# Kernel tuning notes

Measured on AMD Instinct MI355X. Metric: run time of the kernel, lower is better.

## Reference

```python
import jax, jax.numpy as jnp
import numpy as np


def setup_inputs() -> dict:
    key = jax.random.key(0)
    k1, k2 = jax.random.split(key)
    B, P, N, M = 8, 32, 1024, 1024
    normalized_receptive_fields = jax.random.normal(k1, (B, P, N, 3), dtype=jnp.float32)
    reconstructed_points = jax.random.normal(k2, (B, P, M, 3), dtype=jnp.float32)
    return {
        "normalized_receptive_fields": normalized_receptive_fields,
        "reconstructed_points": reconstructed_points,
    }


def reference(normalized_receptive_fields, reconstructed_points):
    B, P, M, _ = reconstructed_points.shape
    N = normalized_receptive_fields.shape[2]
    # Faithful to torch: permute(0,1,3,2) then reshape(-1, M, 3).
    x = jnp.transpose(reconstructed_points, (0, 1, 3, 2)).reshape(-1, M, 3)  # (BP, M, 3)
    y = normalized_receptive_fields.reshape(-1, N, 3)                        # (BP, N, 3)
    xx = jnp.sum(x * x, axis=-1)                 # (BP, M)
    yy = jnp.sum(y * y, axis=-1)                 # (BP, N)
    xy = jnp.einsum('bmc,bnc->bmn', x, y)        # (BP, M, N)
    dist = xx[:, :, None] + yy[:, None, :] - 2.0 * xy  # (BP, M, N)
    min_x_to_y = jnp.min(dist, axis=2)           # (BP, M)
    min_y_to_x = jnp.min(dist, axis=1)           # (BP, N)
    return jnp.mean(min_x_to_y) + jnp.mean(min_y_to_x)
```

## Files before the change

### kernel.cpp

```cpp
#include <hip/hip_runtime.h>


#define MM 1024
#define NN 1024
#define THREADS 1024
#define NWAVES 16
#define FINF 3.4e38f

typedef float f32x4 __attribute__((ext_vector_type(4)));
typedef __bf16 bf16x8 __attribute__((ext_vector_type(8)));

#define BT_OFF 0
#define CK_OFF 65536
#define RS_OFF (CK_OFF + 8192)
#define LDS_BYTES (RS_OFF + 64)

__device__ __forceinline__ unsigned short bf16_rne(float v) {
    unsigned u = __float_as_uint(v);
    u = u + 0x7FFFu + ((u >> 16) & 1u);
    return (unsigned short)(u >> 16);
}
__device__ __forceinline__ float bf16f(unsigned short h) {
    return __uint_as_float(((unsigned)h) << 16);
}
struct S3 { unsigned short h0, h1, h2; };
__device__ __forceinline__ S3 split3(float v) {
    S3 o;
    o.h0 = bf16_rne(v);
    float r = v - bf16f(o.h0);
    o.h1 = bf16_rne(r);
    float r2 = r - bf16f(o.h1);
    o.h2 = bf16_rne(r2);
    return o;
}
__device__ __forceinline__ unsigned pk(unsigned short a, unsigned short b) {
    return (unsigned)a | ((unsigned)b << 16);
}
__device__ __forceinline__ float min3f(float a, float b, float c) {
    return fminf(fminf(a, b), c);
}
template <int CTRL>
__device__ __forceinline__ float dpp_ror_min(float v) {
    int vi = __float_as_int(v);
    int t  = __builtin_amdgcn_update_dpp(vi, vi, CTRL, 0xf, 0xf, true);
    return fminf(v, __int_as_float(t));
}
__device__ __forceinline__ unsigned fkey(float v) {
    unsigned u = __float_as_uint(v);
    return ((int)u < 0) ? ~u : (u | 0x80000000u);
}
__device__ __forceinline__ float unkey(unsigned k) {
    return ((int)k < 0) ? __uint_as_float(k & 0x7FFFFFFFu) : __uint_as_float(~k);
}

__global__ __launch_bounds__(THREADS, 8)
void chamfer_main(const float* __restrict__ nrf,
                  const float* __restrict__ rp,
                  float* __restrict__ colP,
                  float* __restrict__ out,
                  float inv_bpm) {
    __shared__ __align__(16) unsigned char smem[LDS_BYTES];
    unsigned* colK = (unsigned*)(smem + CK_OFF);
    float* rowsumS = (float*)(smem + RS_OFF);

    const int bp   = blockIdx.x >> 1;
    const int half = blockIdx.x & 1;
    const int tid  = threadIdx.x;
    const int lane = tid & 63;
    const int wave = tid >> 6;
    const int l15  = lane & 15;
    const int g    = lane >> 4;
    const unsigned short ONE = 0x3F80;

    const float* yB = nrf + (size_t)bp * NN * 3;
    const float* xB = rp + (size_t)bp * MM * 3;

    {
        const int c = tid;
        float y0 = yB[c * 3 + 0], y1 = yB[c * 3 + 1], y2 = yB[c * 3 + 2];
        float yy = __builtin_fmaf(y0, y0, __builtin_fmaf(y1, y1, y2 * y2));
        S3 b0 = split3(y0), b1 = split3(y1), b2 = split3(y2), q = split3(yy);
        uint4* dst = (uint4*)(smem + BT_OFF + (c >> 4) * 1024 + (c & 15) * 64);
        dst[0] = make_uint4(pk(b0.h0, b0.h1), pk(b0.h0, b0.h1), pk(b0.h2, b0.h0), pk(b1.h0, b1.h1));
        dst[1] = make_uint4(pk(b1.h0, b1.h1), pk(b1.h2, b1.h0), pk(b2.h0, b2.h1), pk(b2.h0, b2.h1));
        dst[2] = make_uint4(pk(b2.h2, b2.h0), pk(ONE, ONE), pk(ONE, q.h0), pk(q.h1, q.h2));
        dst[3] = make_uint4(pk(b0.h2, b0.h1), pk(b1.h2, b1.h1), pk(b2.h2, b2.h1), 0u);
        colK[c] = 0xFFFFFFFFu;
        colK[1024 + c] = 0xFFFFFFFFu;
    }

    bf16x8 af[2];
    #pragma unroll
    for (int s = 0; s < 2; ++s) {
        const int m = half * 512 + wave * 32 + s * 16 + l15;
        const int k = 3 * m;
        float x0 = xB[((k    ) & (MM - 1)) * 3 + ((k    ) >> 10)];
        float x1 = xB[((k + 1) & (MM - 1)) * 3 + ((k + 1) >> 10)];
        float x2 = xB[((k + 2) & (MM - 1)) * 3 + ((k + 2) >> 10)];
        float xx = __builtin_fmaf(x0, x0, __builtin_fmaf(x1, x1, x2 * x2));
        S3 a0 = split3(-2.0f * x0), a1 = split3(-2.0f * x1), a2 = split3(-2.0f * x2);
        S3 p = split3(xx);
        uint4 q0 = make_uint4(pk(a0.h0, a0.h0), pk(a0.h1, a0.h1), pk(a0.h0, a0.h2), pk(a1.h0, a1.h0));
        uint4 q1 = make_uint4(pk(a1.h1, a1.h1), pk(a1.h0, a1.h2), pk(a2.h0, a2.h0), pk(a2.h1, a2.h1));
        uint4 q2 = make_uint4(pk(a2.h0, a2.h2), pk(p.h0, p.h1), pk(p.h2, ONE), pk(ONE, ONE));
        uint4 q3 = make_uint4(pk(a0.h1, a0.h2), pk(a1.h1, a1.h2), pk(a2.h1, a2.h2), 0u);
        uint4 sel = (g == 0) ? q0 : (g == 1) ? q1 : (g == 2) ? q2 : q3;
        union { uint4 u; bf16x8 b; } cv; cv.u = sel;
        af[s] = cv.b;
    }
    __syncthreads();

    const unsigned fragoff = (unsigned)((l15 * 4 + g) * 16);
    const unsigned char* BtBase = smem + BT_OFF;
    unsigned* colKme = colK + (lane >> 5) * 1024 + l15;
    const f32x4 Z = {0.0f, 0.0f, 0.0f, 0.0f};

    float rmin0[4], rmin1[4];
    #pragma unroll
    for (int j = 0; j < 4; ++j) { rmin0[j] = FINF; rmin1[j] = FINF; }

    bf16x8 bfc = *(const bf16x8*)(BtBase + fragoff);
    #pragma unroll
    for (int t = 0; t < 64; ++t) {
        bf16x8 bfn = *(const bf16x8*)(BtBase + (t + 1) * 1024 + fragoff);

        f32x4 acc0 = __builtin_amdgcn_mfma_f32_16x16x32_bf16(af[0], bfc, Z, 0, 0, 0);
        f32x4 acc1 = __builtin_amdgcn_mfma_f32_16x16x32_bf16(af[1], bfc, Z, 0, 0, 0);

        #pragma unroll
        for (int j = 0; j < 4; ++j) rmin0[j] = fminf(rmin0[j], acc0[j]);
        #pragma unroll
        for (int j = 0; j < 4; ++j) rmin1[j] = fminf(rmin1[j], acc1[j]);

        float cm0 = fminf(min3f(acc0[0], acc0[1], acc0[2]), acc0[3]);
        float cm1 = fminf(min3f(acc1[0], acc1[1], acc1[2]), acc1[3]);
        float cm = fminf(cm0, cm1);
        int sw = __builtin_amdgcn_ds_swizzle(__float_as_int(cm), 0x401F);
        cm = fminf(cm, __int_as_float(sw));
        atomicMin(colKme + t * 16, fkey(cm));

        bfc = bfn;
    }

    float rowsum = 0.0f;
    #pragma unroll
    for (int s = 0; s < 2; ++s) {
        #pragma unroll
        for (int j = 0; j < 4; ++j) {
            float v = (s == 0) ? rmin0[j] : rmin1[j];
            v = dpp_ror_min<0x121>(v);
            v = dpp_ror_min<0x122>(v);
            v = dpp_ror_min<0x124>(v);
            v = dpp_ror_min<0x128>(v);
            rowsum += v;
        }
    }
    rowsum += __int_as_float(__builtin_amdgcn_ds_swizzle(__float_as_int(rowsum), 0x401F));
    rowsum += __int_as_float(__builtin_amdgcn_ds_bpermute((lane ^ 32) << 2, __float_as_int(rowsum)));
    if (lane == 0) rowsumS[wave] = rowsum;
    __syncthreads();

    {
        unsigned k0 = colK[tid], k1 = colK[1024 + tid];
        colP[(size_t)blockIdx.x * 1024 + tid] = unkey(k0 < k1 ? k0 : k1);
    }
    if (tid < 64) {
        float r = (tid < 16) ? rowsumS[tid] : 0.0f;
        #pragma unroll
        for (int off = 8; off > 0; off >>= 1) r += __shfl_xor(r, off, 64);
        if (tid == 0) atomicAdd(out, r * inv_bpm);
    }
}

__global__ __launch_bounds__(1024)
void chamfer_reduce(const float* __restrict__ colP, float* __restrict__ out,
                    float inv_bpn) {
    const int bp = blockIdx.x;
    const int tid = threadIdx.x;
    const int lane = tid & 63;
    const int wave = tid >> 6;
    __shared__ float ws[16];

    float v = fminf(colP[(size_t)(2 * bp) * 1024 + tid],
                    colP[(size_t)(2 * bp + 1) * 1024 + tid]);
    #pragma unroll
    for (int off = 32; off > 0; off >>= 1) v += __shfl_xor(v, off, 64);
    if (lane == 0) ws[wave] = v;
    __syncthreads();
    if (tid == 0) {
        float s = 0.0f;
        #pragma unroll
        for (int w = 0; w < 16; ++w) s += ws[w];
        atomicAdd(out, s * inv_bpn);
    }
}

extern "C" void kernel_launch(void* const* d_in, const int* in_sizes, int n_in,
                              void* d_out, int out_size, void* d_ws, size_t ws_size,
                              hipStream_t stream) {
    const float* nrf = (const float*)d_in[0];
    const float* rp  = (const float*)d_in[1];
    float* out = (float*)d_out;
    float* colP = (float*)d_ws;

    const int BP = in_sizes[1] / (MM * 3);
    const float inv_bpm = 1.0f / (float)(BP * MM);
    const float inv_bpn = 1.0f / (float)(BP * NN);

    (void)hipMemsetAsync(out, 0, sizeof(float), stream);
    chamfer_main<<<BP * 2, THREADS, 0, stream>>>(nrf, rp, colP, out, inv_bpm);
    chamfer_reduce<<<BP, 1024, 0, stream>>>(colP, out, inv_bpn);
}
```

Before: 89.45 us.

## Compute both chamfer directions as row-min passes and drop column atomics and reduce kernel

Instead of splitting the M rows across two blocks and tracking column minima with LDS atomicMin, each block pair now computes one direction: block 0 does rows of x against y, block 1 does rows of y against x, each using only register row-min reductions. This removes the per-tile swizzle and atomicMin on LDS, the colP workspace round-trip, and the second reduce kernel launch. In exchange it doubles the total MFMA work, since each distance matrix is computed twice, and raises register use with four A fragments per wave.

New measurement: 126.8 us. 41.7% more time.

```diff
diff --git a/kernel.cpp b/kernel.cpp
--- a/kernel.cpp
+++ b/kernel.cpp
@@ -11,8 +11,8 @@
 typedef __bf16 bf16x8 __attribute__((ext_vector_type(8)));
 
 #define BT_OFF 0
-#define CK_OFF 65536
-#define RS_OFF (CK_OFF + 8192)
+#define PAD_OFF 65536
+#define RS_OFF (PAD_OFF + 1024)
 #define LDS_BYTES (RS_OFF + 64)
 
 __device__ __forceinline__ unsigned short bf16_rne(float v) {
@@ -36,35 +36,23 @@
 __device__ __forceinline__ unsigned pk(unsigned short a, unsigned short b) {
     return (unsigned)a | ((unsigned)b << 16);
 }
-__device__ __forceinline__ float min3f(float a, float b, float c) {
-    return fminf(fminf(a, b), c);
-}
 template <int CTRL>
 __device__ __forceinline__ float dpp_ror_min(float v) {
     int vi = __float_as_int(v);
     int t  = __builtin_amdgcn_update_dpp(vi, vi, CTRL, 0xf, 0xf, true);
     return fminf(v, __int_as_float(t));
 }
-__device__ __forceinline__ unsigned fkey(float v) {
-    unsigned u = __float_as_uint(v);
-    return ((int)u < 0) ? ~u : (u | 0x80000000u);
-}
-__device__ __forceinline__ float unkey(unsigned k) {
-    return ((int)k < 0) ? __uint_as_float(k & 0x7FFFFFFFu) : __uint_as_float(~k);
-}
 
 __global__ __launch_bounds__(THREADS, 8)
 void chamfer_main(const float* __restrict__ nrf,
                   const float* __restrict__ rp,
-                  float* __restrict__ colP,
                   float* __restrict__ out,
-                  float inv_bpm) {
+                  float inv_bpm, float inv_bpn) {
     __shared__ __align__(16) unsigned char smem[LDS_BYTES];
-    unsigned* colK = (unsigned*)(smem + CK_OFF);
     float* rowsumS = (float*)(smem + RS_OFF);
 
     const int bp   = blockIdx.x >> 1;
-    const int half = blockIdx.x & 1;
+    const int dir  = blockIdx.x & 1;
     const int tid  = threadIdx.x;
     const int lane = tid & 63;
     const int wave = tid >> 6;
@@ -77,29 +65,40 @@
 
     {
         const int c = tid;
-        float y0 = yB[c * 3 + 0], y1 = yB[c * 3 + 1], y2 = yB[c * 3 + 2];
-        float yy = __builtin_fmaf(y0, y0, __builtin_fmaf(y1, y1, y2 * y2));
-        S3 b0 = split3(y0), b1 = split3(y1), b2 = split3(y2), q = split3(yy);
+        float v0, v1, v2;
+        if (dir == 0) {
+            v0 = yB[c * 3 + 0]; v1 = yB[c * 3 + 1]; v2 = yB[c * 3 + 2];
+        } else {
+            const int k = 3 * c;
+            v0 = xB[((k    ) & (MM - 1)) * 3 + ((k    ) >> 10)];
+            v1 = xB[((k + 1) & (MM - 1)) * 3 + ((k + 1) >> 10)];
+            v2 = xB[((k + 2) & (MM - 1)) * 3 + ((k + 2) >> 10)];
+        }
+        float nn = __builtin_fmaf(v0, v0, __builtin_fmaf(v1, v1, v2 * v2));
+        S3 b0 = split3(v0), b1 = split3(v1), b2 = split3(v2), q = split3(nn);
         uint4* dst = (uint4*)(smem + BT_OFF + (c >> 4) * 1024 + (c & 15) * 64);
         dst[0] = make_uint4(pk(b0.h0, b0.h1), pk(b0.h0, b0.h1), pk(b0.h2, b0.h0), pk(b1.h0, b1.h1));
         dst[1] = make_uint4(pk(b1.h0, b1.h1), pk(b1.h2, b1.h0), pk(b2.h0, b2.h1), pk(b2.h0, b2.h1));
         dst[2] = make_uint4(pk(b2.h2, b2.h0), pk(ONE, ONE), pk(ONE, q.h0), pk(q.h1, q.h2));
         dst[3] = make_uint4(pk(b0.h2, b0.h1), pk(b1.h2, b1.h1), pk(b2.h2, b2.h1), 0u);
-        colK[c] = 0xFFFFFFFFu;
-        colK[1024 + c] = 0xFFFFFFFFu;
     }
 
-    bf16x8 af[2];
+    bf16x8 af[4];
     #pragma unroll
-    for (int s = 0; s < 2; ++s) {
-        const int m = half * 512 + wave * 32 + s * 16 + l15;
-        const int k = 3 * m;
-        float x0 = xB[((k    ) & (MM - 1)) * 3 + ((k    ) >> 10)];
-        float x1 = xB[((k + 1) & (MM - 1)) * 3 + ((k + 1) >> 10)];
-        float x2 = xB[((k + 2) & (MM - 1)) * 3 + ((k + 2) >> 10)];
-        float xx = __builtin_fmaf(x0, x0, __builtin_fmaf(x1, x1, x2 * x2));
-        S3 a0 = split3(-2.0f * x0), a1 = split3(-2.0f * x1), a2 = split3(-2.0f * x2);
-        S3 p = split3(xx);
+    for (int s = 0; s < 4; ++s) {
+        const int m = wave * 64 + s * 16 + l15;
+        float v0, v1, v2;
+        if (dir == 0) {
+            const int k = 3 * m;
+            v0 = xB[((k    ) & (MM - 1)) * 3 + ((k    ) >> 10)];
+            v1 = xB[((k + 1) & (MM - 1)) * 3 + ((k + 1) >> 10)];
+            v2 = xB[((k + 2) & (MM - 1)) * 3 + ((k + 2) >> 10)];
+        } else {
+            v0 = yB[m * 3 + 0]; v1 = yB[m * 3 + 1]; v2 = yB[m * 3 + 2];
+        }
+        float nn = __builtin_fmaf(v0, v0, __builtin_fmaf(v1, v1, v2 * v2));
+        S3 a0 = split3(-2.0f * v0), a1 = split3(-2.0f * v1), a2 = split3(-2.0f * v2);
+        S3 p = split3(nn);
         uint4 q0 = make_uint4(pk(a0.h0, a0.h0), pk(a0.h1, a0.h1), pk(a0.h0, a0.h2), pk(a1.h0, a1.h0));
         uint4 q1 = make_uint4(pk(a1.h1, a1.h1), pk(a1.h0, a1.h2), pk(a2.h0, a2.h0), pk(a2.h1, a2.h1));
         uint4 q2 = make_uint4(pk(a2.h0, a2.h2), pk(p.h0, p.h1), pk(p.h2, ONE), pk(ONE, ONE));
@@ -110,44 +109,41 @@
     }
     __syncthreads();
 
-    const unsigned fragoff = (unsigned)((l15 * 4 + g) * 16);
-    const unsigned char* BtBase = smem + BT_OFF;
-    unsigned* colKme = colK + (lane >> 5) * 1024 + l15;
+    const unsigned char* BtBase = smem + BT_OFF + (unsigned)((l15 * 4 + g) * 16);
     const f32x4 Z = {0.0f, 0.0f, 0.0f, 0.0f};
 
-    float rmin0[4], rmin1[4];
+    float rmin[4][4];
     #pragma unroll
-    for (int j = 0; j < 4; ++j) { rmin0[j] = FINF; rmin1[j] = FINF; }
+    for (int s = 0; s < 4; ++s)
+        #pragma unroll
+        for (int j = 0; j < 4; ++j) rmin[s][j] = FINF;
 
-    bf16x8 bfc = *(const bf16x8*)(BtBase + fragoff);
+    bf16x8 bfc = *(const bf16x8*)(BtBase);
     #pragma unroll
     for (int t = 0; t < 64; ++t) {
-        bf16x8 bfn = *(const bf16x8*)(BtBase + (t + 1) * 1024 + fragoff);
+        bf16x8 bfn = *(const bf16x8*)(BtBase + (t + 1) * 1024);
 
         f32x4 acc0 = __builtin_amdgcn_mfma_f32_16x16x32_bf16(af[0], bfc, Z, 0, 0, 0);
         f32x4 acc1 = __builtin_amdgcn_mfma_f32_16x16x32_bf16(af[1], bfc, Z, 0, 0, 0);
+        f32x4 acc2 = __builtin_amdgcn_mfma_f32_16x16x32_bf16(af[2], bfc, Z, 0, 0, 0);
+        f32x4 acc3 = __builtin_amdgcn_mfma_f32_16x16x32_bf16(af[3], bfc, Z, 0, 0, 0);
 
         #pragma unroll
-        for (int j = 0; j < 4; ++j) rmin0[j] = fminf(rmin0[j], acc0[j]);
-        #pragma unroll
-        for (int j = 0; j < 4; ++j) rmin1[j] = fminf(rmin1[j], acc1[j]);
-
-        float cm0 = fminf(min3f(acc0[0], acc0[1], acc0[2]), acc0[3]);
-        float cm1 = fminf(min3f(acc1[0], acc1[1], acc1[2]), acc1[3]);
-        float cm = fminf(cm0, cm1);
-        int sw = __builtin_amdgcn_ds_swizzle(__float_as_int(cm), 0x401F);
-        cm = fminf(cm, __int_as_float(sw));
-        atomicMin(colKme + t * 16, fkey(cm));
-
+        for (int j = 0; j < 4; ++j) {
+            rmin[0][j] = fminf(rmin[0][j], acc0[j]);
+            rmin[1][j] = fminf(rmin[1][j], acc1[j]);
+            rmin[2][j] = fminf(rmin[2][j], acc2[j]);
+            rmin[3][j] = fminf(rmin[3][j], acc3[j]);
+        }
         bfc = bfn;
     }
 
     float rowsum = 0.0f;
     #pragma unroll
-    for (int s = 0; s < 2; ++s) {
+    for (int s = 0; s < 4; ++s) {
         #pragma unroll
         for (int j = 0; j < 4; ++j) {
-            float v = (s == 0) ? rmin0[j] : rmin1[j];
+            float v = rmin[s][j];
             v = dpp_ror_min<0x121>(v);
             v = dpp_ror_min<0x122>(v);
             v = dpp_ror_min<0x124>(v);
@@ -160,38 +156,11 @@
     if (lane == 0) rowsumS[wave] = rowsum;
     __syncthreads();
 
-    {
-        unsigned k0 = colK[tid], k1 = colK[1024 + tid];
-        colP[(size_t)blockIdx.x * 1024 + tid] = unkey(k0 < k1 ? k0 : k1);
-    }
     if (tid < 64) {
-        float r = (tid < 16) ? rowsumS[tid] : 0.0f;
+        float r = (tid < NWAVES) ? rowsumS[tid] : 0.0f;
         #pragma unroll
         for (int off = 8; off > 0; off >>= 1) r += __shfl_xor(r, off, 64);
-        if (tid == 0) atomicAdd(out, r * inv_bpm);
-    }
-}
-
-__global__ __launch_bounds__(1024)
-void chamfer_reduce(const float* __restrict__ colP, float* __restrict__ out,
-                    float inv_bpn) {
-    const int bp = blockIdx.x;
-    const int tid = threadIdx.x;
-    const int lane = tid & 63;
-    const int wave = tid >> 6;
-    __shared__ float ws[16];
-
-    float v = fminf(colP[(size_t)(2 * bp) * 1024 + tid],
-                    colP[(size_t)(2 * bp + 1) * 1024 + tid]);
-    #pragma unroll
-    for (int off = 32; off > 0; off >>= 1) v += __shfl_xor(v, off, 64);
-    if (lane == 0) ws[wave] = v;
-    __syncthreads();
-    if (tid == 0) {
-        float s = 0.0f;
-        #pragma unroll
-        for (int w = 0; w < 16; ++w) s += ws[w];
-        atomicAdd(out, s * inv_bpn);
+        if (tid == 0) atomicAdd(out, r * (dir ? inv_bpn : inv_bpm));
     }
 }
 
@@ -201,13 +170,11 @@
     const float* nrf = (const float*)d_in[0];
     const float* rp  = (const float*)d_in[1];
     float* out = (float*)d_out;
-    float* colP = (float*)d_ws;
 
     const int BP = in_sizes[1] / (MM * 3);
     const float inv_bpm = 1.0f / (float)(BP * MM);
     const float inv_bpn = 1.0f / (float)(BP * NN);
 
     (void)hipMemsetAsync(out, 0, sizeof(float), stream);
-    chamfer_main<<<BP * 2, THREADS, 0, stream>>>(nrf, rp, colP, out, inv_bpm);
-    chamfer_reduce<<<BP, 1024, 0, stream>>>(colP, out, inv_bpn);
+    chamfer_main<<<BP * 2, THREADS, 0, stream>>>(nrf, rp, out, inv_bpm, inv_bpn);
 }
```
